# Kernel optimization log

Measured on AMD Instinct MI355X. Metric: run time of the kernel, lower is better.

## Reference

```python
import jax, jax.numpy as jnp
import numpy as np

B = 64        # graphs per batch
N = 1024      # nodes per graph
DEG = 16      # avg degree
E = B * N * DEG
F_IN = 10
H = 128
NC = 10
K1, K2, K3 = 205, 41, 9   # ceil(0.2 * prev_nodes_per_graph)


def _lin(key, fan_in, shape):
    return jax.random.normal(key, shape, jnp.float32) * (1.0 / np.sqrt(fan_in))


def setup_inputs() -> dict:
    key = jax.random.key(0)
    ks = jax.random.split(key, 32)
    x = jax.random.normal(ks[0], (B * N, F_IN), jnp.float32)
    # random intra-graph edges (source_to_target)
    src_l = jax.random.randint(ks[1], (B, N * DEG), 0, N)
    dst_l = jax.random.randint(ks[2], (B, N * DEG), 0, N)
    off = (jnp.arange(B) * N)[:, None]
    edge_index = jnp.stack([(src_l + off).reshape(-1), (dst_l + off).reshape(-1)]).astype(jnp.int32)
    inp = dict(x=x, edge_index=edge_index)
    inp["W1"] = _lin(ks[3], F_IN, (F_IN, H)); inp["b1"] = jnp.zeros((H,), jnp.float32)
    inp["W2"] = _lin(ks[4], H, (H, H));       inp["b2"] = jnp.zeros((H,), jnp.float32)
    inp["W3"] = _lin(ks[5], H, (H, H));       inp["b3"] = jnp.zeros((H,), jnp.float32)
    inp["Ws1"] = _lin(ks[6], H, (H, 1)); inp["bs1"] = jnp.zeros((1,), jnp.float32)
    inp["Ws2"] = _lin(ks[7], H, (H, 1)); inp["bs2"] = jnp.zeros((1,), jnp.float32)
    inp["Ws3"] = _lin(ks[8], H, (H, 1)); inp["bs3"] = jnp.zeros((1,), jnp.float32)
    inp["Wl1"] = _lin(ks[9], 2 * H, (2 * H, H));    inp["bl1"] = jnp.zeros((H,), jnp.float32)
    inp["Wl2"] = _lin(ks[10], H, (H, H // 2));      inp["bl2"] = jnp.zeros((H // 2,), jnp.float32)
    inp["Wl3"] = _lin(ks[11], H // 2, (H // 2, NC)); inp["bl3"] = jnp.zeros((NC,), jnp.float32)
    return inp


def gcn(x, W, b, src, dst, emask, n):
    """PyG GCNConv: symmetric norm with self-loops; masked edges contribute 0."""
    h = x @ W                                   # [n, out]
    w = emask.astype(h.dtype)                   # edge weights (0 for filtered edges)
    deg = jax.ops.segment_sum(w, dst, num_segments=n) + 1.0   # +1 self-loop
    dis = jax.lax.rsqrt(deg)                    # deg^{-1/2}
    norm = dis[src] * dis[dst] * w              # [E]
    out = jax.ops.segment_sum(h[src] * norm[:, None], dst, num_segments=n)
    out = out + h * (dis * dis)[:, None]        # self-loop message
    return out + b


def sagpool(x, src, dst, emask, Ws, bs, cur, k):
    """SAGPool: GCN score -> per-graph top-k -> gather + tanh gate -> filter_adj."""
    n = B * cur
    score = gcn(x, Ws, bs, src, dst, emask, n)[:, 0]          # [n]
    _, idx = jax.lax.top_k(score.reshape(B, cur), k)          # [B, k]
    perm = (idx + (jnp.arange(B) * cur)[:, None]).reshape(-1) # global node ids
    x = x[perm] * jnp.tanh(score[perm])[:, None]
    # filter_adj: remap node ids, drop edges with an unselected endpoint
    new_id = jnp.full((n,), -1, jnp.int32).at[perm].set(jnp.arange(B * k, dtype=jnp.int32))
    nsrc, ndst = new_id[src], new_id[dst]
    emask = emask & (nsrc >= 0) & (ndst >= 0)
    nsrc = jnp.where(emask, nsrc, 0)
    ndst = jnp.where(emask, ndst, 0)
    return x, nsrc, ndst, emask


def readout(x, k):
    xb = x.reshape(B, k, -1)
    return jnp.concatenate([xb.max(axis=1), xb.mean(axis=1)], axis=1)   # [B, 2H]


def reference(x, edge_index, W1, b1, W2, b2, W3, b3,
              Ws1, bs1, Ws2, bs2, Ws3, bs3,
              Wl1, bl1, Wl2, bl2, Wl3, bl3):
    src, dst = edge_index[0], edge_index[1]
    emask = jnp.ones((E,), bool)

    h = jax.nn.relu(gcn(x, W1, b1, src, dst, emask, B * N))
    h, src, dst, emask = sagpool(h, src, dst, emask, Ws1, bs1, N, K1)
    x1 = readout(h, K1)

    h = jax.nn.relu(gcn(h, W2, b2, src, dst, emask, B * K1))
    h, src, dst, emask = sagpool(h, src, dst, emask, Ws2, bs2, K1, K2)
    x2 = readout(h, K2)

    h = jax.nn.relu(gcn(h, W3, b3, src, dst, emask, B * K2))
    h, src, dst, emask = sagpool(h, src, dst, emask, Ws3, bs3, K2, K3)
    x3 = readout(h, K3)

    z = x1 + x2 + x3                             # [B, 2H]
    z = jax.nn.relu(z @ Wl1 + bl1)               # dropout is eval-mode identity
    z = jax.nn.relu(z @ Wl2 + bl2)
    return jax.nn.log_softmax(z @ Wl3 + bl3, axis=-1)
```

## Files before the change

kernel.cpp:

```cpp
#include <hip/hip_runtime.h>
#include <math.h>

#define NB 64
#define N0 1024
#define NEDGE 1048576
#define EPG 16384
#define FIN 10
#define NCLS 10
#define KP1 205
#define KP2 41
#define KP3 9

static inline int ceil_div(int a, int b) { return (a + b - 1) / b; }

__global__ __launch_bounds__(1024) void build_csr1_k(const int* __restrict__ ei,
                                                     float* __restrict__ disg,
                                                     int* __restrict__ offg,
                                                     int* __restrict__ cntg,
                                                     int2* __restrict__ csr2) {
    __shared__ int cnt[N0];
    __shared__ int cur[N0];
    __shared__ float disl[N0];
    __shared__ int scan[1024];
    int b = blockIdx.x, t = threadIdx.x;
    cnt[t] = 0;
    __syncthreads();
    const int ebase = b * EPG;
    const int nbase = b * N0;
    #pragma unroll
    for (int u = 0; u < EPG / 1024; ++u) {
        int d = ei[NEDGE + ebase + u * 1024 + t] - nbase;
        atomicAdd(&cnt[d], 1);
    }
    __syncthreads();
    int v = cnt[t];
    scan[t] = v;
    __syncthreads();
    #pragma unroll
    for (int s = 1; s < 1024; s <<= 1) {
        int tv = (t >= s) ? scan[t - s] : 0;
        __syncthreads();
        scan[t] += tv;
        __syncthreads();
    }
    int excl = scan[t] - v;
    cur[t] = excl;
    float di = rsqrtf((float)v + 1.0f);
    disl[t] = di;
    offg[nbase + t] = ebase + excl;
    cntg[nbase + t] = v;
    disg[nbase + t] = di;
    __syncthreads();
    #pragma unroll
    for (int u = 0; u < EPG / 1024; ++u) {
        int j = ebase + u * 1024 + t;
        int s = ei[j], d = ei[NEDGE + j] - nbase;
        int pos = atomicAdd(&cur[d], 1);
        int2 o; o.x = s; o.y = __float_as_int(disl[s - nbase]);
        csr2[ebase + pos] = o;
    }
}

__global__ __launch_bounds__(256) void agg10_k(const float* __restrict__ x,
                                               const int2* __restrict__ csr2,
                                               const int* __restrict__ off,
                                               const int* __restrict__ cnt,
                                               const float* __restrict__ dis,
                                               float* __restrict__ y) {
    __shared__ float xl[N0 * 11];
    int b = blockIdx.x >> 2, chunk = blockIdx.x & 3;
    const float* xg = x + (size_t)b * (N0 * FIN);
    for (int u = threadIdx.x; u < N0 * FIN; u += 256) {
        int r = u / FIN, c = u - r * FIN;
        xl[r * 11 + c] = xg[u];
    }
    __syncthreads();
    int li = chunk * 256 + threadIdx.x;
    int i  = b * N0 + li;
    int s0 = off[i], m = cnt[i];
    int base = b * N0;
    float acc[FIN];
    #pragma unroll
    for (int f = 0; f < FIN; ++f) acc[f] = 0.f;
    int j = 0;
    for (; j + 2 <= m; j += 2) {
        int2 e0 = csr2[s0 + j], e1 = csr2[s0 + j + 1];
        int sl0 = (e0.x - base) * 11, sl1 = (e1.x - base) * 11;
        float w0 = __int_as_float(e0.y), w1 = __int_as_float(e1.y);
        #pragma unroll
        for (int f = 0; f < FIN; ++f) acc[f] += xl[sl0 + f] * w0 + xl[sl1 + f] * w1;
    }
    if (j < m) {
        int2 e0 = csr2[s0 + j];
        int sl0 = (e0.x - base) * 11;
        float w0 = __int_as_float(e0.y);
        #pragma unroll
        for (int f = 0; f < FIN; ++f) acc[f] += xl[sl0 + f] * w0;
    }
    float di = dis[i], d2 = di * di;
    #pragma unroll
    for (int f = 0; f < FIN; ++f)
        y[(size_t)i * FIN + f] = di * acc[f] + d2 * xl[li * 11 + f];
}

__global__ void gemm_fin_fused_k(const float* __restrict__ y, const float* __restrict__ W,
                                 const float* __restrict__ bb, const float* __restrict__ Wsc,
                                 const float* __restrict__ dis,
                                 float* __restrict__ hout, float* __restrict__ hs,
                                 float* __restrict__ hsd, int n) {
    __shared__ float Ws[FIN * 128];
    __shared__ float Sc[128];
    for (int u = threadIdx.x; u < FIN * 128; u += 256) Ws[u] = W[u];
    if (threadIdx.x < 128) Sc[threadIdx.x] = Wsc[threadIdx.x];
    __syncthreads();
    int t = blockIdx.x * 256 + threadIdx.x;
    int i = t >> 6, lane = threadIdx.x & 63;
    if (i >= n) return;
    float a = (lane < FIN) ? y[(size_t)i * FIN + lane] : 0.f;
    const float2* W2 = (const float2*)Ws;
    float ax = bb[lane * 2], ay = bb[lane * 2 + 1];
    #pragma unroll
    for (int k = 0; k < FIN; ++k) {
        float ak = __shfl(a, k);
        float2 w = W2[k * 64 + lane];
        ax += ak * w.x; ay += ak * w.y;
    }
    ax = fmaxf(ax, 0.f); ay = fmaxf(ay, 0.f);
    float2 o; o.x = ax; o.y = ay;
    ((float2*)hout)[(size_t)i * 64 + lane] = o;
    float part = ax * Sc[lane * 2] + ay * Sc[lane * 2 + 1];
    #pragma unroll
    for (int sh = 32; sh >= 1; sh >>= 1) part += __shfl_xor(part, sh);
    if (lane == 0) { hs[i] = part; hsd[i] = part * dis[i]; }
}

__global__ __launch_bounds__(1024) void s1_topk_build2_k(
    const float* __restrict__ hout, const float* __restrict__ hs,
    const float* __restrict__ hsd, const int* __restrict__ ei,
    int2* __restrict__ csr,
    const int* __restrict__ off1, const int* __restrict__ cnt1,
    const float* __restrict__ dis1, const float* __restrict__ bs1,
    float* __restrict__ hA, float* __restrict__ z, int* __restrict__ newid1,
    int* __restrict__ off2, int* __restrict__ cnt2g, float* __restrict__ dis2g) {
    __shared__ float v[1024];
    __shared__ int   ix[1024];
    __shared__ float zm[1024];
    __shared__ float zs[1024];
    __shared__ float hl[1024];
    __shared__ int   n1l[1024];
    __shared__ int   c2[KP1];
    __shared__ int   cur2[KP1];
    __shared__ float d2l[KP1];
    __shared__ int   scan[1024];
    int b = blockIdx.x, t = threadIdx.x;
    const int nbase = b * N0, ebase = b * EPG;

    hl[t] = hsd[nbase + t];
    __syncthreads();
    {
        int s0 = off1[nbase + t], e0 = s0 + cnt1[nbase + t];
        float acc = 0.f;
        int j = s0;
        for (; j + 4 <= e0; j += 4) {
            int a0 = csr[j].x, a1 = csr[j+1].x, a2 = csr[j+2].x, a3 = csr[j+3].x;
            acc += hl[a0 - nbase] + hl[a1 - nbase] + hl[a2 - nbase] + hl[a3 - nbase];
        }
        for (; j < e0; ++j) acc += hl[csr[j].x - nbase];
        float di = dis1[nbase + t];
        v[t] = di * acc + hs[nbase + t] * (di * di) + bs1[0];
        ix[t] = t;
    }
    __syncthreads();
    for (int size = 2; size <= 1024; size <<= 1) {
        for (int stride = size >> 1; stride > 0; stride >>= 1) {
            if (t < 512) {
                int pos = 2 * t - (t & (stride - 1));
                int j2 = pos + stride;
                bool asc = (pos & size) == 0;
                float v0 = v[pos], v1 = v[j2];
                int i0 = ix[pos], i1 = ix[j2];
                bool jb = (v1 > v0) || (v1 == v0 && i1 < i0);
                bool sw = asc ? jb : !jb;
                if (sw) { v[pos] = v1; v[j2] = v0; ix[pos] = i1; ix[j2] = i0; }
            }
            __syncthreads();
        }
    }
    {
        int node = ix[t];
        int loc = (t < KP1) ? t : -1;
        n1l[node] = loc;
        newid1[nbase + node] = (t < KP1) ? (b * KP1 + t) : -1;
        if (t < KP1) zm[t] = tanhf(v[t]);
    }
    __syncthreads();
    {
        int g = t >> 7, f = t & 127;
        float vmax = -INFINITY, vsum = 0.f;
        for (int j = g; j < KP1; j += 8) {
            int src = nbase + ix[j];
            float val = hout[(size_t)src * 128 + f] * zm[j];
            hA[((size_t)b * KP1 + j) * 128 + f] = val;
            vmax = fmaxf(vmax, val); vsum += val;
        }
        __syncthreads();
        zm[t] = vmax; zs[t] = vsum;
        __syncthreads();
        if (t < 128) {
            float m = zm[t], s2 = zs[t];
            #pragma unroll
            for (int g2 = 1; g2 < 8; ++g2) { m = fmaxf(m, zm[g2 * 128 + t]); s2 += zs[g2 * 128 + t]; }
            z[b * 256 + t] = m;
            z[b * 256 + 128 + t] = s2 / (float)KP1;
        }
    }
    __syncthreads();
    if (t < KP1) c2[t] = 0;
    __syncthreads();
    int sl[EPG / 1024], dl[EPG / 1024];
    #pragma unroll
    for (int u = 0; u < EPG / 1024; ++u) {
        int j = ebase + u * 1024 + t;
        int s = ei[j] - nbase, d = ei[NEDGE + j] - nbase;
        int ls = n1l[s], ld = n1l[d];
        bool alive = (ls >= 0 && ld >= 0);
        sl[u] = alive ? ls : -1; dl[u] = ld;
        if (alive) atomicAdd(&c2[ld], 1);
    }
    __syncthreads();
    int vv = (t < KP1) ? c2[t] : 0;
    scan[t] = vv;
    __syncthreads();
    #pragma unroll
    for (int s = 1; s < 1024; s <<= 1) {
        int tv = (t >= s) ? scan[t - s] : 0;
        __syncthreads();
        scan[t] += tv;
        __syncthreads();
    }
    if (t < KP1) {
        int excl = scan[t] - vv;
        cur2[t] = excl;
        float dd = rsqrtf((float)vv + 1.0f);
        d2l[t] = dd;
        off2[b * KP1 + t] = ebase + excl;
        cnt2g[b * KP1 + t] = vv;
        dis2g[b * KP1 + t] = dd;
    }
    __syncthreads();
    #pragma unroll
    for (int u = 0; u < EPG / 1024; ++u) {
        if (sl[u] < 0) continue;
        int pos = atomicAdd(&cur2[dl[u]], 1);
        int2 o; o.x = b * KP1 + sl[u]; o.y = __float_as_int(d2l[sl[u]]);
        csr[ebase + pos] = o;
    }
}

__global__ __launch_bounds__(256) void gemm128_tiled_k(const float* __restrict__ A,
                                                       const float* __restrict__ W,
                                                       float* __restrict__ C, int n) {
    __shared__ float As[64][33];
    __shared__ float Wt[32][64];
    int tx = threadIdx.x & 15, ty = threadIdx.x >> 4;
    int r0 = blockIdx.x * 64;
    int c0 = blockIdx.y * 64;
    float4 acc0 = {0,0,0,0}, acc1 = {0,0,0,0}, acc2 = {0,0,0,0}, acc3 = {0,0,0,0};
    int u = threadIdx.x;
    for (int k0 = 0; k0 < 128; k0 += 32) {
        __syncthreads();
        {
            int rr = u >> 3, cc = (u & 7) * 4;
            #pragma unroll
            for (int h = 0; h < 2; ++h) {
                int r = rr + h * 32;
                float4 v = {0,0,0,0};
                if (r0 + r < n) v = *(const float4*)&A[(size_t)(r0 + r) * 128 + k0 + cc];
                As[r][cc] = v.x; As[r][cc+1] = v.y; As[r][cc+2] = v.z; As[r][cc+3] = v.w;
            }
        }
        {
            int kk = u >> 4, c = (u & 15) * 4;
            #pragma unroll
            for (int h = 0; h < 2; ++h) {
                float4 v = *(const float4*)&W[(size_t)(k0 + kk + h * 16) * 128 + c0 + c];
                *(float4*)&Wt[kk + h * 16][c] = v;
            }
        }
        __syncthreads();
        #pragma unroll
        for (int kk = 0; kk < 32; ++kk) {
            float4 wv = *(const float4*)&Wt[kk][tx * 4];
            float a0 = As[ty * 4 + 0][kk];
            float a1 = As[ty * 4 + 1][kk];
            float a2 = As[ty * 4 + 2][kk];
            float a3 = As[ty * 4 + 3][kk];
            acc0.x += a0 * wv.x; acc0.y += a0 * wv.y; acc0.z += a0 * wv.z; acc0.w += a0 * wv.w;
            acc1.x += a1 * wv.x; acc1.y += a1 * wv.y; acc1.z += a1 * wv.z; acc1.w += a1 * wv.w;
            acc2.x += a2 * wv.x; acc2.y += a2 * wv.y; acc2.z += a2 * wv.z; acc2.w += a2 * wv.w;
            acc3.x += a3 * wv.x; acc3.y += a3 * wv.y; acc3.z += a3 * wv.z; acc3.w += a3 * wv.w;
        }
    }
    int r = r0 + ty * 4;
    if (r + 0 < n) *(float4*)&C[(size_t)(r + 0) * 128 + c0 + tx * 4] = acc0;
    if (r + 1 < n) *(float4*)&C[(size_t)(r + 1) * 128 + c0 + tx * 4] = acc1;
    if (r + 2 < n) *(float4*)&C[(size_t)(r + 2) * 128 + c0 + tx * 4] = acc2;
    if (r + 3 < n) *(float4*)&C[(size_t)(r + 3) * 128 + c0 + tx * 4] = acc3;
}

__global__ void gcn_agg_fused2_k(const float* __restrict__ hW, const int2* __restrict__ csr2,
                                 const int* __restrict__ off, const int* __restrict__ cnt,
                                 const float* __restrict__ dis, const float* __restrict__ bias,
                                 const float* __restrict__ Wsc,
                                 float* __restrict__ hout, float* __restrict__ hs,
                                 float* __restrict__ hsd, int n, int cpx) {
    int wg = ((blockIdx.x & 7) * cpx) + (blockIdx.x >> 3);
    int t = wg * blockDim.x + threadIdx.x;
    int i = t >> 6;
    int lane = threadIdx.x & 63;
    if (i >= n) return;
    const float2* hW2 = (const float2*)hW;
    int s0 = off[i], e0 = s0 + cnt[i];
    float accx = 0.f, accy = 0.f;
    for (int j0 = s0; j0 < e0; j0 += 64) {
        int rem = e0 - j0;
        int m = rem < 64 ? rem : 64;
        int sv = 0; float wv = 0.f;
        if (lane < m) { int2 ec = csr2[j0 + lane]; sv = ec.x; wv = __int_as_float(ec.y); }
        int u = 0;
        for (; u + 4 <= m; u += 4) {
            int a0 = __shfl(sv, u + 0), a1 = __shfl(sv, u + 1);
            int a2 = __shfl(sv, u + 2), a3 = __shfl(sv, u + 3);
            float w0 = __shfl(wv, u + 0), w1 = __shfl(wv, u + 1);
            float w2 = __shfl(wv, u + 2), w3 = __shfl(wv, u + 3);
            float2 v0 = hW2[(size_t)a0 * 64 + lane];
            float2 v1 = hW2[(size_t)a1 * 64 + lane];
            float2 v2 = hW2[(size_t)a2 * 64 + lane];
            float2 v3 = hW2[(size_t)a3 * 64 + lane];
            accx += v0.x * w0 + v1.x * w1 + v2.x * w2 + v3.x * w3;
            accy += v0.y * w0 + v1.y * w1 + v2.y * w2 + v3.y * w3;
        }
        for (; u < m; ++u) {
            int s = __shfl(sv, u);
            float w = __shfl(wv, u);
            float2 v = hW2[(size_t)s * 64 + lane];
            accx += v.x * w; accy += v.y * w;
        }
    }
    float di = dis[i];
    float2 hv = hW2[(size_t)i * 64 + lane];
    float ox = fmaxf(di * accx + hv.x * (di * di) + bias[lane * 2], 0.f);
    float oy = fmaxf(di * accy + hv.y * (di * di) + bias[lane * 2 + 1], 0.f);
    float2 o; o.x = ox; o.y = oy;
    ((float2*)hout)[(size_t)i * 64 + lane] = o;
    float part = ox * Wsc[lane * 2] + oy * Wsc[lane * 2 + 1];
    #pragma unroll
    for (int sh = 32; sh >= 1; sh >>= 1) part += __shfl_xor(part, sh);
    if (lane == 0) { hs[i] = part; hsd[i] = part * di; }
}

__global__ __launch_bounds__(1024) void s2_topk_build3_k(
    const float* __restrict__ hout, const float* __restrict__ hs,
    const float* __restrict__ hsd, const int* __restrict__ ei,
    int2* __restrict__ csr,
    const int* __restrict__ off2, const int* __restrict__ cnt2,
    const float* __restrict__ dis2, const float* __restrict__ bs2,
    const int* __restrict__ newid1,
    float* __restrict__ hA, float* __restrict__ z,
    int* __restrict__ off3, int* __restrict__ cnt3g, float* __restrict__ dis3g) {
    __shared__ float v[256];
    __shared__ int   ix[256];
    __shared__ float hl[256];
    __shared__ float zm[1024];
    __shared__ float zs[1024];
    __shared__ int   n1g[1024];
    __shared__ int   n2l[KP1];
    __shared__ int   c3[KP2];
    __shared__ int   cur3[KP2];
    __shared__ float d3l[KP2];
    __shared__ int   scan[1024];
    int b = blockIdx.x, t = threadIdx.x;
    const int nbase = b * N0, ebase = b * EPG;

    if (t < KP1) hl[t] = hsd[b * KP1 + t];
    { int g1 = newid1[nbase + t]; n1g[t] = (g1 >= 0) ? (g1 - b * KP1) : -1; }
    __syncthreads();
    float sc = -INFINITY;
    if (t < KP1) {
        int i = b * KP1 + t;
        int s0 = off2[i], e0 = s0 + cnt2[i];
        float acc = 0.f;
        int j = s0;
        for (; j + 4 <= e0; j += 4) {
            int a0 = csr[j].x, a1 = csr[j+1].x, a2 = csr[j+2].x, a3 = csr[j+3].x;
            acc += hl[a0 - b*KP1] + hl[a1 - b*KP1] + hl[a2 - b*KP1] + hl[a3 - b*KP1];
        }
        for (; j < e0; ++j) acc += hl[csr[j].x - b*KP1];
        float di = dis2[i];
        sc = di * acc + hs[i] * (di * di) + bs2[0];
    }
    if (t < 256) { v[t] = sc; ix[t] = t; }
    __syncthreads();
    for (int size = 2; size <= 256; size <<= 1) {
        for (int stride = size >> 1; stride > 0; stride >>= 1) {
            if (t < 128) {
                int pos = 2 * t - (t & (stride - 1));
                int j2 = pos + stride;
                bool asc = (pos & size) == 0;
                float v0 = v[pos], v1 = v[j2];
                int i0 = ix[pos], i1 = ix[j2];
                bool jb = (v1 > v0) || (v1 == v0 && i1 < i0);
                bool sw = asc ? jb : !jb;
                if (sw) { v[pos] = v1; v[j2] = v0; ix[pos] = i1; ix[j2] = i0; }
            }
            __syncthreads();
        }
    }
    if (t < 256) { int node = ix[t]; if (node < KP1) n2l[node] = (t < KP2) ? t : -1; }
    if (t < KP2) zm[t] = tanhf(v[t]);
    __syncthreads();
    {
        int g = t >> 7, f = t & 127;
        float vmax = -INFINITY, vsum = 0.f;
        for (int j = g; j < KP2; j += 8) {
            int src = b * KP1 + ix[j];
            float val = hout[(size_t)src * 128 + f] * zm[j];
            hA[((size_t)b * KP2 + j) * 128 + f] = val;
            vmax = fmaxf(vmax, val); vsum += val;
        }
        __syncthreads();
        zm[t] = vmax; zs[t] = vsum;
        __syncthreads();
        if (t < 128) {
            float m = zm[t], s2 = zs[t];
            #pragma unroll
            for (int g2 = 1; g2 < 8; ++g2) { m = fmaxf(m, zm[g2 * 128 + t]); s2 += zs[g2 * 128 + t]; }
            z[b * 256 + t] += m;
            z[b * 256 + 128 + t] += s2 / (float)KP2;
        }
    }
    __syncthreads();
    if (t < KP2) c3[t] = 0;
    __syncthreads();
    int sl[EPG / 1024], dl[EPG / 1024];
    #pragma unroll
    for (int u = 0; u < EPG / 1024; ++u) {
        int j = ebase + u * 1024 + t;
        int s = ei[j] - nbase, d = ei[NEDGE + j] - nbase;
        int a = n1g[s], bb = n1g[d];
        int ls = -1, ld = -1;
        if (a >= 0 && bb >= 0) { ls = n2l[a]; ld = n2l[bb]; }
        bool alive = (ls >= 0 && ld >= 0);
        sl[u] = alive ? ls : -1; dl[u] = ld;
        if (alive) atomicAdd(&c3[ld], 1);
    }
    __syncthreads();
    int vv = (t < KP2) ? c3[t] : 0;
    scan[t] = vv;
    __syncthreads();
    #pragma unroll
    for (int s = 1; s < 1024; s <<= 1) {
        int tv = (t >= s) ? scan[t - s] : 0;
        __syncthreads();
        scan[t] += tv;
        __syncthreads();
    }
    if (t < KP2) {
        int excl = scan[t] - vv;
        cur3[t] = excl;
        float dd = rsqrtf((float)vv + 1.0f);
        d3l[t] = dd;
        off3[b * KP2 + t] = ebase + excl;
        cnt3g[b * KP2 + t] = vv;
        dis3g[b * KP2 + t] = dd;
    }
    __syncthreads();
    #pragma unroll
    for (int u = 0; u < EPG / 1024; ++u) {
        if (sl[u] < 0) continue;
        int pos = atomicAdd(&cur3[dl[u]], 1);
        int2 o; o.x = b * KP2 + sl[u]; o.y = __float_as_int(d3l[sl[u]]);
        csr[ebase + pos] = o;
    }
}

__global__ __launch_bounds__(128) void s3_topk_mlp_k(
    const float* __restrict__ hout, const float* __restrict__ hs,
    const float* __restrict__ hsd, const int2* __restrict__ csr,
    const int* __restrict__ off3, const int* __restrict__ cnt3,
    const float* __restrict__ dis3, const float* __restrict__ bs3,
    const float* __restrict__ z,
    const float* __restrict__ Wl1, const float* __restrict__ bl1,
    const float* __restrict__ Wl2, const float* __restrict__ bl2,
    const float* __restrict__ Wl3, const float* __restrict__ bl3,
    float* __restrict__ out) {
    __shared__ float hl[KP2];
    __shared__ float v[64];
    __shared__ int   ix[64];
    __shared__ float zm[KP3];
    __shared__ float zr[256], h1[128], h2[64], lg[NCLS], red[2];
    int b = blockIdx.x, t = threadIdx.x;

    if (t < KP2) hl[t] = hsd[b * KP2 + t];
    __syncthreads();
    float sc = -INFINITY;
    if (t < KP2) {
        int i = b * KP2 + t;
        int s0 = off3[i], e0 = s0 + cnt3[i];
        float acc = 0.f;
        for (int j = s0; j < e0; ++j) acc += hl[csr[j].x - b*KP2];
        float di = dis3[i];
        sc = di * acc + hs[i] * (di * di) + bs3[0];
    }
    if (t < 64) { v[t] = sc; ix[t] = t; }
    __syncthreads();
    for (int size = 2; size <= 64; size <<= 1) {
        for (int stride = size >> 1; stride > 0; stride >>= 1) {
            if (t < 32) {
                int pos = 2 * t - (t & (stride - 1));
                int j2 = pos + stride;
                bool asc = (pos & size) == 0;
                float v0 = v[pos], v1 = v[j2];
                int i0 = ix[pos], i1 = ix[j2];
                bool jb = (v1 > v0) || (v1 == v0 && i1 < i0);
                bool sw = asc ? jb : !jb;
                if (sw) { v[pos] = v1; v[j2] = v0; ix[pos] = i1; ix[j2] = i0; }
            }
            __syncthreads();
        }
    }
    if (t < KP3) zm[t] = tanhf(v[t]);
    __syncthreads();
    {
        float vmax = -INFINITY, vsum = 0.f;
        #pragma unroll
        for (int j = 0; j < KP3; ++j) {
            int src = b * KP2 + ix[j];
            float val = hout[(size_t)src * 128 + t] * zm[j];
            vmax = fmaxf(vmax, val); vsum += val;
        }
        zr[t] = z[b * 256 + t] + vmax;
        zr[128 + t] = z[b * 256 + 128 + t] + vsum / (float)KP3;
    }
    __syncthreads();
    float acc = bl1[t];
    #pragma unroll 8
    for (int i = 0; i < 256; ++i) acc += zr[i] * Wl1[i * 128 + t];
    h1[t] = fmaxf(acc, 0.f);
    __syncthreads();
    if (t < 64) {
        float a2 = bl2[t];
        #pragma unroll 8
        for (int i = 0; i < 128; ++i) a2 += h1[i] * Wl2[i * 64 + t];
        h2[t] = fmaxf(a2, 0.f);
    }
    __syncthreads();
    if (t < NCLS) {
        float a3 = bl3[t];
        #pragma unroll 8
        for (int i = 0; i < 64; ++i) a3 += h2[i] * Wl3[i * NCLS + t];
        lg[t] = a3;
    }
    __syncthreads();
    if (t == 0) {
        float m = lg[0];
        for (int i = 1; i < NCLS; ++i) m = fmaxf(m, lg[i]);
        float s = 0.f;
        for (int i = 0; i < NCLS; ++i) s += expf(lg[i] - m);
        red[0] = m; red[1] = logf(s);
    }
    __syncthreads();
    if (t < NCLS) out[b * NCLS + t] = lg[t] - red[0] - red[1];
}

extern "C" void kernel_launch(void* const* d_in, const int* in_sizes, int n_in,
                              void* d_out, int out_size, void* d_ws, size_t ws_size,
                              hipStream_t stream) {
    const float* x   = (const float*)d_in[0];
    const int*   ei  = (const int*)d_in[1];
    const float* W1  = (const float*)d_in[2];  const float* b1  = (const float*)d_in[3];
    const float* W2  = (const float*)d_in[4];  const float* b2  = (const float*)d_in[5];
    const float* W3  = (const float*)d_in[6];  const float* b3  = (const float*)d_in[7];
    const float* Ws1 = (const float*)d_in[8];  const float* bs1 = (const float*)d_in[9];
    const float* Ws2 = (const float*)d_in[10]; const float* bs2 = (const float*)d_in[11];
    const float* Ws3 = (const float*)d_in[12]; const float* bs3 = (const float*)d_in[13];
    const float* Wl1 = (const float*)d_in[14]; const float* bl1 = (const float*)d_in[15];
    const float* Wl2 = (const float*)d_in[16]; const float* bl2 = (const float*)d_in[17];
    const float* Wl3 = (const float*)d_in[18]; const float* bl3 = (const float*)d_in[19];
    float* out = (float*)d_out;

    const int NMAX = NB * N0;
    const int N1 = NB * KP1;
    const int N2 = NB * KP2;

    char* p = (char*)d_ws;
    float* z      = (float*)p; p += (size_t)NB * 256 * 4;
    float* hW     = (float*)p; p += (size_t)N1 * 128 * 4;
    float* hout   = (float*)p; p += (size_t)NMAX * 128 * 4;
    float* hA     = (float*)p; p += (size_t)N1 * 128 * 4;
    float* y      = (float*)p; p += (size_t)NMAX * FIN * 4;
    float* dis1   = (float*)p; p += (size_t)NMAX * 4;
    float* hs     = (float*)p; p += (size_t)NMAX * 4;
    float* hsd    = (float*)p; p += (size_t)NMAX * 4;
    int* newid1   = (int*)p;   p += (size_t)NMAX * 4;
    int* off1     = (int*)p;   p += (size_t)NMAX * 4;
    int* cnt1     = (int*)p;   p += (size_t)NMAX * 4;
    int* off2     = (int*)p;   p += (size_t)N1 * 4;
    int* cnt2     = (int*)p;   p += (size_t)N1 * 4;
    float* dis2   = (float*)p; p += (size_t)N1 * 4;
    int* off3     = (int*)p;   p += (size_t)N2 * 4;
    int* cnt3     = (int*)p;   p += (size_t)N2 * 4;
    float* dis3   = (float*)p; p += (size_t)N2 * 4;
    int2* csr2    = (int2*)p;  p += (size_t)NEDGE * 8;

    build_csr1_k<<<NB, 1024, 0, stream>>>(ei, dis1, off1, cnt1, csr2);
    agg10_k<<<NB * 4, 256, 0, stream>>>(x, csr2, off1, cnt1, dis1, y);
    gemm_fin_fused_k<<<NMAX / 4, 256, 0, stream>>>(y, W1, b1, Ws1, dis1, hout, hs, hsd, NMAX);
    s1_topk_build2_k<<<NB, 1024, 0, stream>>>(hout, hs, hsd, ei, csr2, off1, cnt1, dis1,
                                              bs1, hA, z, newid1, off2, cnt2, dis2);

    {
        dim3 g(ceil_div(N1, 64), 2);
        gemm128_tiled_k<<<g, 256, 0, stream>>>(hA, W2, hW, N1);
    }
    gcn_agg_fused2_k<<<N1 / 4, 256, 0, stream>>>(
        hW, csr2, off2, cnt2, dis2, b2, Ws2, hout, hs, hsd, N1, N1 / 32);
    s2_topk_build3_k<<<NB, 1024, 0, stream>>>(hout, hs, hsd, ei, csr2, off2, cnt2, dis2,
                                              bs2, newid1, hA, z, off3, cnt3, dis3);

    {
        dim3 g(ceil_div(N2, 64), 2);
        gemm128_tiled_k<<<g, 256, 0, stream>>>(hA, W3, hW, N2);
    }
    gcn_agg_fused2_k<<<N2 / 4, 256, 0, stream>>>(
        hW, csr2, off3, cnt3, dis3, b3, Ws3, hout, hs, hsd, N2, N2 / 32);
    s3_topk_mlp_k<<<NB, 128, 0, stream>>>(hout, hs, hsd, csr2, off3, cnt3, dis3, bs3, z,
                                          Wl1, bl1, Wl2, bl2, Wl3, bl3, out);
}
```

Baseline: 271.7 us.

## Replace bitonic top-k with radix select, wave-shuffle scans, compact stage-2 edge list

Swaps the full bitonic sort used for top-k in the pooling kernels for a bitwise radix select on order-preserving float keys, followed by stable compaction through prefix scans. Replaces the shared-memory Hillis-Steele block scans with a wave-shuffle two-level scan, which needs far fewer barriers. Stage 2 now reads a compacted surviving-edge list (csr plus a new dst array and per-graph edge count) written by stage 1, instead of rescanning all 16K original edges per graph. Selected nodes come out in index order rather than score order, which changes the row order of the pooled tensor; the max and mean readouts do not depend on that order. The cost is an extra dst2 write of one int per surviving edge.

```diff
diff --git a/kernel.cpp b/kernel.cpp
--- a/kernel.cpp
+++ b/kernel.cpp
@@ -13,6 +13,28 @@
 
 static inline int ceil_div(int a, int b) { return (a + b - 1) / b; }
 
+__device__ __forceinline__ int block_scan_incl(int v, int* wtot, int lane, int wid) {
+    __syncthreads();
+    int x = v;
+    #pragma unroll
+    for (int s = 1; s < 64; s <<= 1) { int tv = __shfl_up(x, s); if (lane >= s) x += tv; }
+    if (lane == 63) wtot[wid] = x;
+    __syncthreads();
+    if (wid == 0) {
+        int w = (lane < 16) ? wtot[lane] : 0;
+        #pragma unroll
+        for (int s = 1; s < 16; s <<= 1) { int tv = __shfl_up(w, s); if (lane >= s) w += tv; }
+        if (lane < 16) wtot[lane] = w;
+    }
+    __syncthreads();
+    return x + ((wid > 0) ? wtot[wid - 1] : 0);
+}
+
+__device__ __forceinline__ unsigned fkey(float f) {
+    unsigned b = __float_as_uint(f);
+    return (f >= 0.f) ? (b | 0x80000000u) : ~b;
+}
+
 __global__ __launch_bounds__(1024) void build_csr1_k(const int* __restrict__ ei,
                                                      float* __restrict__ disg,
                                                      int* __restrict__ offg,
@@ -21,8 +43,9 @@
     __shared__ int cnt[N0];
     __shared__ int cur[N0];
     __shared__ float disl[N0];
-    __shared__ int scan[1024];
+    __shared__ int wtot[16];
     int b = blockIdx.x, t = threadIdx.x;
+    int lane = t & 63, wid = t >> 6;
     cnt[t] = 0;
     __syncthreads();
     const int ebase = b * EPG;
@@ -34,16 +57,8 @@
     }
     __syncthreads();
     int v = cnt[t];
-    scan[t] = v;
-    __syncthreads();
-    #pragma unroll
-    for (int s = 1; s < 1024; s <<= 1) {
-        int tv = (t >= s) ? scan[t - s] : 0;
-        __syncthreads();
-        scan[t] += tv;
-        __syncthreads();
-    }
-    int excl = scan[t] - v;
+    int inc = block_scan_incl(v, wtot, lane, wid);
+    int excl = inc - v;
     cur[t] = excl;
     float di = rsqrtf((float)v + 1.0f);
     disl[t] = di;
@@ -141,22 +156,27 @@
     const int* __restrict__ off1, const int* __restrict__ cnt1,
     const float* __restrict__ dis1, const float* __restrict__ bs1,
     float* __restrict__ hA, float* __restrict__ z, int* __restrict__ newid1,
-    int* __restrict__ off2, int* __restrict__ cnt2g, float* __restrict__ dis2g) {
-    __shared__ float v[1024];
-    __shared__ int   ix[1024];
+    int* __restrict__ off2, int* __restrict__ cnt2g, float* __restrict__ dis2g,
+    int* __restrict__ dst2, int* __restrict__ etot2) {
+    __shared__ float hl[1024];
+    __shared__ unsigned u[1024];
+    __shared__ int wtot[16];
+    __shared__ unsigned tinfo[2];
+    __shared__ int   n1l[1024];
+    __shared__ int   seln[KP1];
+    __shared__ float gatel[KP1];
     __shared__ float zm[1024];
     __shared__ float zs[1024];
-    __shared__ float hl[1024];
-    __shared__ int   n1l[1024];
     __shared__ int   c2[KP1];
     __shared__ int   cur2[KP1];
     __shared__ float d2l[KP1];
-    __shared__ int   scan[1024];
     int b = blockIdx.x, t = threadIdx.x;
+    int lane = t & 63, wid = t >> 6;
     const int nbase = b * N0, ebase = b * EPG;
 
     hl[t] = hsd[nbase + t];
     __syncthreads();
+    float sc;
     {
         int s0 = off1[nbase + t], e0 = s0 + cnt1[nbase + t];
         float acc = 0.f;
@@ -167,43 +187,48 @@
         }
         for (; j < e0; ++j) acc += hl[csr[j].x - nbase];
         float di = dis1[nbase + t];
-        v[t] = di * acc + hs[nbase + t] * (di * di) + bs1[0];
-        ix[t] = t;
-    }
-    __syncthreads();
-    for (int size = 2; size <= 1024; size <<= 1) {
-        for (int stride = size >> 1; stride > 0; stride >>= 1) {
-            if (t < 512) {
-                int pos = 2 * t - (t & (stride - 1));
-                int j2 = pos + stride;
-                bool asc = (pos & size) == 0;
-                float v0 = v[pos], v1 = v[j2];
-                int i0 = ix[pos], i1 = ix[j2];
-                bool jb = (v1 > v0) || (v1 == v0 && i1 < i0);
-                bool sw = asc ? jb : !jb;
-                if (sw) { v[pos] = v1; v[j2] = v0; ix[pos] = i1; ix[j2] = i0; }
-            }
-            __syncthreads();
-        }
-    }
-    {
-        int node = ix[t];
-        int loc = (t < KP1) ? t : -1;
-        n1l[node] = loc;
-        newid1[nbase + node] = (t < KP1) ? (b * KP1 + t) : -1;
-        if (t < KP1) zm[t] = tanhf(v[t]);
+        sc = di * acc + hs[nbase + t] * (di * di) + bs1[0];
+    }
+    unsigned kb = fkey(sc);
+    u[t] = kb;
+    __syncthreads();
+    if (wid == 0) {
+        int remaining = KP1; unsigned prefix = 0;
+        for (int bit = 31; bit >= 0; --bit) {
+            int c = 0;
+            #pragma unroll 4
+            for (int i = lane; i < 1024; i += 64)
+                c += ((u[i] >> bit) == ((prefix >> bit) | 1u));
+            #pragma unroll
+            for (int s = 32; s >= 1; s >>= 1) c += __shfl_xor(c, s);
+            if (c >= remaining) prefix |= (1u << bit);
+            else remaining -= c;
+        }
+        if (lane == 0) { tinfo[0] = prefix; tinfo[1] = (unsigned)remaining; }
+    }
+    __syncthreads();
+    unsigned T = tinfo[0]; int extra = (int)tinfo[1];
+    int gt = (kb > T), eq = (kb == T);
+    int eqIncl = block_scan_incl(eq, wtot, lane, wid);
+    int sel = gt || (eq && (eqIncl - eq) < extra);
+    int selIncl = block_scan_incl(sel, wtot, lane, wid);
+    int loc = selIncl - sel;
+    if (sel) {
+        n1l[t] = loc; seln[loc] = t; gatel[loc] = tanhf(sc);
+        newid1[nbase + t] = b * KP1 + loc;
+    } else {
+        n1l[t] = -1; newid1[nbase + t] = -1;
     }
     __syncthreads();
     {
         int g = t >> 7, f = t & 127;
         float vmax = -INFINITY, vsum = 0.f;
         for (int j = g; j < KP1; j += 8) {
-            int src = nbase + ix[j];
-            float val = hout[(size_t)src * 128 + f] * zm[j];
+            int src = nbase + seln[j];
+            float val = hout[(size_t)src * 128 + f] * gatel[j];
             hA[((size_t)b * KP1 + j) * 128 + f] = val;
             vmax = fmaxf(vmax, val); vsum += val;
         }
-        __syncthreads();
         zm[t] = vmax; zs[t] = vsum;
         __syncthreads();
         if (t < 128) {
@@ -217,29 +242,18 @@
     __syncthreads();
     if (t < KP1) c2[t] = 0;
     __syncthreads();
-    int sl[EPG / 1024], dl[EPG / 1024];
-    #pragma unroll
-    for (int u = 0; u < EPG / 1024; ++u) {
-        int j = ebase + u * 1024 + t;
+    #pragma unroll
+    for (int uu = 0; uu < EPG / 1024; ++uu) {
+        int j = ebase + uu * 1024 + t;
         int s = ei[j] - nbase, d = ei[NEDGE + j] - nbase;
         int ls = n1l[s], ld = n1l[d];
-        bool alive = (ls >= 0 && ld >= 0);
-        sl[u] = alive ? ls : -1; dl[u] = ld;
-        if (alive) atomicAdd(&c2[ld], 1);
+        if (ls >= 0 && ld >= 0) atomicAdd(&c2[ld], 1);
     }
     __syncthreads();
     int vv = (t < KP1) ? c2[t] : 0;
-    scan[t] = vv;
-    __syncthreads();
-    #pragma unroll
-    for (int s = 1; s < 1024; s <<= 1) {
-        int tv = (t >= s) ? scan[t - s] : 0;
-        __syncthreads();
-        scan[t] += tv;
-        __syncthreads();
-    }
+    int inc = block_scan_incl(vv, wtot, lane, wid);
+    int excl = inc - vv;
     if (t < KP1) {
-        int excl = scan[t] - vv;
         cur2[t] = excl;
         float dd = rsqrtf((float)vv + 1.0f);
         d2l[t] = dd;
@@ -247,13 +261,18 @@
         cnt2g[b * KP1 + t] = vv;
         dis2g[b * KP1 + t] = dd;
     }
-    __syncthreads();
-    #pragma unroll
-    for (int u = 0; u < EPG / 1024; ++u) {
-        if (sl[u] < 0) continue;
-        int pos = atomicAdd(&cur2[dl[u]], 1);
-        int2 o; o.x = b * KP1 + sl[u]; o.y = __float_as_int(d2l[sl[u]]);
+    if (t == 1023) etot2[b] = inc;
+    __syncthreads();
+    #pragma unroll
+    for (int uu = 0; uu < EPG / 1024; ++uu) {
+        int j = ebase + uu * 1024 + t;
+        int s = ei[j] - nbase, d = ei[NEDGE + j] - nbase;
+        int ls = n1l[s], ld = n1l[d];
+        if (ls < 0 || ld < 0) continue;
+        int pos = atomicAdd(&cur2[ld], 1);
+        int2 o; o.x = b * KP1 + ls; o.y = __float_as_int(d2l[ls]);
         csr[ebase + pos] = o;
+        dst2[ebase + pos] = ld;
     }
 }
 
@@ -361,29 +380,29 @@
 
 __global__ __launch_bounds__(1024) void s2_topk_build3_k(
     const float* __restrict__ hout, const float* __restrict__ hs,
-    const float* __restrict__ hsd, const int* __restrict__ ei,
-    int2* __restrict__ csr,
+    const float* __restrict__ hsd,
+    int2* __restrict__ csr, const int* __restrict__ dst2, const int* __restrict__ etot2,
     const int* __restrict__ off2, const int* __restrict__ cnt2,
     const float* __restrict__ dis2, const float* __restrict__ bs2,
-    const int* __restrict__ newid1,
     float* __restrict__ hA, float* __restrict__ z,
     int* __restrict__ off3, int* __restrict__ cnt3g, float* __restrict__ dis3g) {
-    __shared__ float v[256];
-    __shared__ int   ix[256];
     __shared__ float hl[256];
+    __shared__ unsigned u2[256];
+    __shared__ int wtot[16];
+    __shared__ unsigned tinfo[2];
+    __shared__ int   n2l[KP1];
+    __shared__ int   seln[KP2];
+    __shared__ float gatel[KP2];
     __shared__ float zm[1024];
     __shared__ float zs[1024];
-    __shared__ int   n1g[1024];
-    __shared__ int   n2l[KP1];
     __shared__ int   c3[KP2];
     __shared__ int   cur3[KP2];
     __shared__ float d3l[KP2];
-    __shared__ int   scan[1024];
     int b = blockIdx.x, t = threadIdx.x;
-    const int nbase = b * N0, ebase = b * EPG;
+    int lane = t & 63, wid = t >> 6;
+    const int ebase = b * EPG;
 
     if (t < KP1) hl[t] = hsd[b * KP1 + t];
-    { int g1 = newid1[nbase + t]; n1g[t] = (g1 >= 0) ? (g1 - b * KP1) : -1; }
     __syncthreads();
     float sc = -INFINITY;
     if (t < KP1) {
@@ -399,36 +418,45 @@
         float di = dis2[i];
         sc = di * acc + hs[i] * (di * di) + bs2[0];
     }
-    if (t < 256) { v[t] = sc; ix[t] = t; }
-    __syncthreads();
-    for (int size = 2; size <= 256; size <<= 1) {
-        for (int stride = size >> 1; stride > 0; stride >>= 1) {
-            if (t < 128) {
-                int pos = 2 * t - (t & (stride - 1));
-                int j2 = pos + stride;
-                bool asc = (pos & size) == 0;
-                float v0 = v[pos], v1 = v[j2];
-                int i0 = ix[pos], i1 = ix[j2];
-                bool jb = (v1 > v0) || (v1 == v0 && i1 < i0);
-                bool sw = asc ? jb : !jb;
-                if (sw) { v[pos] = v1; v[j2] = v0; ix[pos] = i1; ix[j2] = i0; }
-            }
-            __syncthreads();
-        }
-    }
-    if (t < 256) { int node = ix[t]; if (node < KP1) n2l[node] = (t < KP2) ? t : -1; }
-    if (t < KP2) zm[t] = tanhf(v[t]);
+    unsigned kb = fkey(sc);
+    if (t < 256) u2[t] = kb;
+    __syncthreads();
+    if (wid == 0) {
+        int remaining = KP2; unsigned prefix = 0;
+        for (int bit = 31; bit >= 0; --bit) {
+            int c = 0;
+            #pragma unroll
+            for (int i = lane; i < 256; i += 64)
+                c += ((u2[i] >> bit) == ((prefix >> bit) | 1u));
+            #pragma unroll
+            for (int s = 32; s >= 1; s >>= 1) c += __shfl_xor(c, s);
+            if (c >= remaining) prefix |= (1u << bit);
+            else remaining -= c;
+        }
+        if (lane == 0) { tinfo[0] = prefix; tinfo[1] = (unsigned)remaining; }
+    }
+    __syncthreads();
+    unsigned T = tinfo[0]; int extra = (int)tinfo[1];
+    int valid = (t < KP1);
+    int gt = valid && (kb > T), eq = valid && (kb == T);
+    int eqIncl = block_scan_incl(eq, wtot, lane, wid);
+    int sel = gt || (eq && (eqIncl - eq) < extra);
+    int selIncl = block_scan_incl(sel, wtot, lane, wid);
+    int loc = selIncl - sel;
+    if (valid) {
+        if (sel) { n2l[t] = loc; seln[loc] = t; gatel[loc] = tanhf(sc); }
+        else     n2l[t] = -1;
+    }
     __syncthreads();
     {
         int g = t >> 7, f = t & 127;
         float vmax = -INFINITY, vsum = 0.f;
         for (int j = g; j < KP2; j += 8) {
-            int src = b * KP1 + ix[j];
-            float val = hout[(size_t)src * 128 + f] * zm[j];
+            int src = b * KP1 + seln[j];
+            float val = hout[(size_t)src * 128 + f] * gatel[j];
             hA[((size_t)b * KP2 + j) * 128 + f] = val;
             vmax = fmaxf(vmax, val); vsum += val;
         }
-        __syncthreads();
         zm[t] = vmax; zs[t] = vsum;
         __syncthreads();
         if (t < 128) {
@@ -440,33 +468,31 @@
         }
     }
     __syncthreads();
+    int nE2 = etot2[b];
+    int es[2], ed[2];
+    #pragma unroll
+    for (int r = 0; r < 2; ++r) {
+        int i = r * 1024 + t;
+        if (i < nE2) { es[r] = csr[ebase + i].x - b * KP1; ed[r] = dst2[ebase + i]; }
+        else es[r] = -1;
+    }
+    __syncthreads();
     if (t < KP2) c3[t] = 0;
     __syncthreads();
-    int sl[EPG / 1024], dl[EPG / 1024];
-    #pragma unroll
-    for (int u = 0; u < EPG / 1024; ++u) {
-        int j = ebase + u * 1024 + t;
-        int s = ei[j] - nbase, d = ei[NEDGE + j] - nbase;
-        int a = n1g[s], bb = n1g[d];
-        int ls = -1, ld = -1;
-        if (a >= 0 && bb >= 0) { ls = n2l[a]; ld = n2l[bb]; }
-        bool alive = (ls >= 0 && ld >= 0);
-        sl[u] = alive ? ls : -1; dl[u] = ld;
-        if (alive) atomicAdd(&c3[ld], 1);
+    int ms[2], md[2];
+    #pragma unroll
+    for (int r = 0; r < 2; ++r) {
+        ms[r] = -1;
+        if (es[r] >= 0) {
+            int ls = n2l[es[r]], ld = n2l[ed[r]];
+            if (ls >= 0 && ld >= 0) { ms[r] = ls; md[r] = ld; atomicAdd(&c3[ld], 1); }
+        }
     }
     __syncthreads();
     int vv = (t < KP2) ? c3[t] : 0;
-    scan[t] = vv;
-    __syncthreads();
-    #pragma unroll
-    for (int s = 1; s < 1024; s <<= 1) {
-        int tv = (t >= s) ? scan[t - s] : 0;
-        __syncthreads();
-        scan[t] += tv;
-        __syncthreads();
-    }
+    int inc = block_scan_incl(vv, wtot, lane, wid);
+    int excl = inc - vv;
     if (t < KP2) {
-        int excl = scan[t] - vv;
         cur3[t] = excl;
         float dd = rsqrtf((float)vv + 1.0f);
         d3l[t] = dd;
@@ -476,10 +502,10 @@
     }
     __syncthreads();
     #pragma unroll
-    for (int u = 0; u < EPG / 1024; ++u) {
-        if (sl[u] < 0) continue;
-        int pos = atomicAdd(&cur3[dl[u]], 1);
-        int2 o; o.x = b * KP2 + sl[u]; o.y = __float_as_int(d3l[sl[u]]);
+    for (int r = 0; r < 2; ++r) {
+        if (ms[r] < 0) continue;
+        int pos = atomicAdd(&cur3[md[r]], 1);
+        int2 o; o.x = b * KP2 + ms[r]; o.y = __float_as_int(d3l[ms[r]]);
         csr[ebase + pos] = o;
     }
 }
@@ -611,13 +637,16 @@
     int* off3     = (int*)p;   p += (size_t)N2 * 4;
     int* cnt3     = (int*)p;   p += (size_t)N2 * 4;
     float* dis3   = (float*)p; p += (size_t)N2 * 4;
+    int* dst2     = (int*)p;   p += (size_t)NEDGE * 4;
+    int* etot2    = (int*)p;   p += (size_t)NB * 4;
     int2* csr2    = (int2*)p;  p += (size_t)NEDGE * 8;
 
     build_csr1_k<<<NB, 1024, 0, stream>>>(ei, dis1, off1, cnt1, csr2);
     agg10_k<<<NB * 4, 256, 0, stream>>>(x, csr2, off1, cnt1, dis1, y);
     gemm_fin_fused_k<<<NMAX / 4, 256, 0, stream>>>(y, W1, b1, Ws1, dis1, hout, hs, hsd, NMAX);
     s1_topk_build2_k<<<NB, 1024, 0, stream>>>(hout, hs, hsd, ei, csr2, off1, cnt1, dis1,
-                                              bs1, hA, z, newid1, off2, cnt2, dis2);
+                                              bs1, hA, z, newid1, off2, cnt2, dis2,
+                                              dst2, etot2);
 
     {
         dim3 g(ceil_div(N1, 64), 2);
@@ -625,8 +654,9 @@
     }
     gcn_agg_fused2_k<<<N1 / 4, 256, 0, stream>>>(
         hW, csr2, off2, cnt2, dis2, b2, Ws2, hout, hs, hsd, N1, N1 / 32);
-    s2_topk_build3_k<<<NB, 1024, 0, stream>>>(hout, hs, hsd, ei, csr2, off2, cnt2, dis2,
-                                              bs2, newid1, hA, z, off3, cnt3, dis3);
+    s2_topk_build3_k<<<NB, 1024, 0, stream>>>(hout, hs, hsd, csr2, dst2, etot2,
+                                              off2, cnt2, dis2, bs2, hA, z,
+                                              off3, cnt3, dis3);
 
     {
         dim3 g(ceil_div(N2, 64), 2);
```

Measured after the change: 271.2 us. Within noise of the previous version (-0.2%).
